# Performance work log

Hardware: AMD Instinct MI355X
Metric: run time of the kernel (lower is better)

Reference implementation:

```python
import jax, jax.numpy as jnp
import numpy as np

C = 768
HEADS = 12
NF = 8      # num_frames
SL = 196    # seq_len (patches per frame)
B = 2
N = 1 + NF * SL
HID = 4 * C


def _ln(x, g, b, eps=1e-5):
    mu = jnp.mean(x, axis=-1, keepdims=True)
    var = jnp.mean((x - mu) ** 2, axis=-1, keepdims=True)
    return (x - mu) * jax.lax.rsqrt(var + eps) * g + b


def setup_inputs() -> dict:
    key = jax.random.key(0)
    ks = jax.random.split(key, 16)
    s = 0.02
    return {
        "x": jax.random.normal(ks[0], (B, N, C), jnp.float32),
        "g1": jnp.ones((C,), jnp.float32),
        "b1": jnp.zeros((C,), jnp.float32),
        "Wqkv": jax.random.normal(ks[1], (C, 3 * C), jnp.float32) * s,
        "Wq": jax.random.normal(ks[2], (C, C), jnp.float32) * s,
        "Wkv": jax.random.normal(ks[3], (C, 2 * C), jnp.float32) * s,
        "Wp": jax.random.normal(ks[4], (C, C), jnp.float32) * s,
        "bp": jnp.zeros((C,), jnp.float32),
        "g2": jnp.ones((C,), jnp.float32),
        "b2": jnp.zeros((C,), jnp.float32),
        "W1": jax.random.normal(ks[5], (C, HID), jnp.float32) * s,
        "bf1": jnp.zeros((HID,), jnp.float32),
        "W2": jax.random.normal(ks[6], (HID, C), jnp.float32) * s,
        "bf2": jnp.zeros((C,), jnp.float32),
        "seq_len": SL,
        "num_frames": NF,
    }


def _traj_attn(xn, Wqkv, Wq, Wkv, Wp, bp, P, F):
    Bb, Nn, Cc = xn.shape
    h = HEADS
    d = Cc // h
    scale = d ** -0.5
    S = F * P  # non-cls tokens

    qkv = xn @ Wqkv                                   # (B,N,3C)
    q, k, v = jnp.split(qkv, 3, axis=-1)

    def heads(t):  # (B,N,C) -> (B*h, N, d)
        return t.reshape(Bb, Nn, h, d).transpose(0, 2, 1, 3).reshape(Bb * h, Nn, d)

    q, k, v = heads(q), heads(k), heads(v)
    cls_q, q_ = q[:, :1], q[:, 1:]
    k_ = k[:, 1:]
    v_ = v[:, 1:]

    # cls token attends to all tokens
    sim = jnp.einsum('bid,bjd->bij', cls_q * scale, k)
    cls_out = jnp.einsum('bij,bjd->bid', jax.nn.softmax(sim, axis=-1), v)
    cls_out = cls_out.reshape(Bb, h, 1, d).transpose(0, 2, 1, 3).reshape(Bb, 1, Cc)

    # stage 1: space-only softmax per frame
    qk = jnp.einsum('bqd,bkd->bqk', q_, k_).reshape(Bb * h, S, F, P)
    space_attn = jax.nn.softmax(scale * qk, axis=-1)          # (Bh,S,F,P)
    v_r = v_.reshape(Bb * h, F, P, d)
    x1 = jnp.einsum('bqfn,bfnd->bqfd', space_attn, v_r)       # (Bh,S,F,d)
    x1 = x1.reshape(Bb, h, S, F, d).transpose(0, 2, 3, 1, 4).reshape(Bb, S, F, Cc)

    # diagonal across (query-frame, key-frame)
    xg = x1.reshape(Bb, F, P, F, Cc)
    diag = jnp.diagonal(xg, axis1=1, axis2=3)                 # (B,P,C,F)
    x_diag = diag.transpose(0, 3, 1, 2).reshape(Bb, S, Cc)    # b (f n) d

    # stage 2: frame-wise attention
    q2 = (x_diag @ Wq).reshape(Bb, S, h, d).transpose(0, 2, 1, 3) * scale  # bhsd
    kv2 = x1 @ Wkv
    k2, v2 = jnp.split(kv2, 2, axis=-1)
    k2 = k2.reshape(Bb, S, F, h, d).transpose(0, 3, 1, 2, 4)  # bhsfd
    attn2 = jax.nn.softmax(jnp.einsum('bhsd,bhsfd->bhsf', q2, k2), axis=-1)
    xo = x1.reshape(Bb, S, F, h, d).transpose(0, 3, 1, 2, 4)  # use_original_code=True
    out = jnp.einsum('bhsf,bhsfd->bhsd', attn2, xo)
    out = out.transpose(0, 2, 1, 3).reshape(Bb, S, Cc)

    out = jnp.concatenate([cls_out, out], axis=1) @ Wp + bp
    return out


def reference(x, g1, b1, Wqkv, Wq, Wkv, Wp, bp, g2, b2, W1, bf1, W2, bf2, seq_len, num_frames):
    x = x + _traj_attn(_ln(x, g1, b1), Wqkv, Wq, Wkv, Wp, bp, seq_len, num_frames)
    h = _ln(x, g2, b2)
    h = jax.nn.gelu(h @ W1 + bf1, approximate=False) @ W2 + bf2
    return x + h
```

## Files before the change

kernel.cpp:

```cpp
#include <hip/hip_runtime.h>
#include <hip/hip_bf16.h>
#include <math.h>

#define C     768
#define HEADS 12
#define HD    64
#define NF    8
#define SL    196
#define BB    2
#define NN    1569
#define SS    1568
#define HID   3072
#define CLS_CH 256
#define CLS_NC 7
#define QSCALE 0.18033688011112042f

typedef __attribute__((ext_vector_type(8))) short short8;
typedef __attribute__((ext_vector_type(4))) float f32x4;
typedef unsigned short u16;

__device__ inline float fast_exp2(float x) { return __builtin_amdgcn_exp2f(x); }

__device__ inline u16 f2b(float f) {
    __hip_bfloat16 h = __float2bfloat16(f);
    return *reinterpret_cast<u16*>(&h);
}
__device__ inline float b2f(u16 u) {
    union { unsigned u; float f; } v; v.u = ((unsigned)u) << 16;
    return v.f;
}

__device__ inline void gload_lds16(const void* g, void* l) {
    __builtin_amdgcn_global_load_lds(
        (const __attribute__((address_space(1))) void*)g,
        (__attribute__((address_space(3))) void*)l, 16, 0, 0);
}

__global__ void ln_kernel(const float* __restrict__ x, const float* __restrict__ g,
                          const float* __restrict__ b, u16* __restrict__ out, int rows) {
    int row = blockIdx.x;
    if (row >= rows) return;
    const float* xr = x + (size_t)row * C;
    int tid = threadIdx.x;
    float v[3];
    float sum = 0.f, sumsq = 0.f;
#pragma unroll
    for (int i = 0; i < 3; i++) {
        v[i] = xr[tid + 256 * i];
        sum += v[i]; sumsq += v[i] * v[i];
    }
    __shared__ float s1[4], s2[4];
    for (int off = 32; off; off >>= 1) {
        sum   += __shfl_xor(sum, off);
        sumsq += __shfl_xor(sumsq, off);
    }
    int wave = tid >> 6, lane = tid & 63;
    if (lane == 0) { s1[wave] = sum; s2[wave] = sumsq; }
    __syncthreads();
    sum   = s1[0] + s1[1] + s1[2] + s1[3];
    sumsq = s2[0] + s2[1] + s2[2] + s2[3];
    float mu  = sum / C;
    float var = sumsq / C - mu * mu;
    float rstd = rsqrtf(fmaxf(var, 0.f) + 1e-5f);
    u16* outr = out + (size_t)row * C;
#pragma unroll
    for (int i = 0; i < 3; i++) {
        int c = tid + 256 * i;
        outr[c] = f2b((v[i] - mu) * rstd * g[c] + b[c]);
    }
}

__global__ void wtrans_kernel(const float* __restrict__ W, u16* __restrict__ Wt,
                              int K, int N, int ldb) {
    __shared__ float tile[64][65];
    int nb = blockIdx.x * 64, kb = blockIdx.y * 64;
    int tx = threadIdx.x & 63, ty = threadIdx.x >> 6;
#pragma unroll
    for (int i = 0; i < 64; i += 4)
        tile[ty + i][tx] = W[(size_t)(kb + ty + i) * ldb + nb + tx];
    __syncthreads();
#pragma unroll
    for (int i = 0; i < 64; i += 4)
        Wt[(size_t)(nb + ty + i) * K + kb + tx] = f2b(tile[tx][ty + i]);
}

template<int MODE, int BM, int BN>
__global__ __launch_bounds__(256) void gemm_bf16(
    const u16* __restrict__ A, const u16* __restrict__ Bt,
    const float* __restrict__ bias, const float* resid, void* Cout,
    int M, int N, int K, int lda, int ldb, int gx) {
    constexpr int MT   = BM / 32;
    constexpr int NT   = BN / 32;
    constexpr int ACH  = BM * 4;
    constexpr int TCH  = (BM + BN) * 4;
    constexpr int HALF = (BM + BN) * 64;
    __shared__ char smem[2 * HALF];
    int tid = threadIdx.x, lane = tid & 63, wave = tid >> 6;
    int wr = wave >> 1, wc = wave & 1;
    int r16 = lane & 15, kg = lane >> 4;

    int nwg = gridDim.x, orig = blockIdx.x;
    int qq = nwg >> 3, rr = nwg & 7, xcd = orig & 7, lid = orig >> 3;
    int wg = (xcd < rr ? xcd * (qq + 1) : rr * (qq + 1) + (xcd - rr) * qq) + lid;
    int bx = wg % gx, by = wg / gx;
    if constexpr (MODE == 4) {
        int mt_ = (M + BM - 1) / BM;
        int chunk = by / mt_; by -= chunk * mt_;
        A    += (size_t)chunk * K;
        Bt   += (size_t)chunk * K;
        Cout  = (void*)((float*)Cout + (size_t)chunk * ((size_t)M * N));
    }
    int row0 = by * BM, col0 = bx * BN;

    f32x4 acc[MT][NT];
#pragma unroll
    for (int mt = 0; mt < MT; mt++)
#pragma unroll
        for (int nt = 0; nt < NT; nt++) acc[mt][nt] = (f32x4){0.f, 0.f, 0.f, 0.f};

    auto stage = [&](char* dstbase, int ks) {
        int k0 = ks << 5;
#pragma unroll
        for (int it = 0; it < TCH / 256; it++) {
            int c = it * 256 + tid;
            const u16* src;
            if (c < ACH) {
                int ml = c >> 2, s = c & 3;
                int kgs = s ^ ((ml >> 1) & 3);
                int gm = row0 + ml; if (gm >= M) gm = M - 1;
                src = A + (size_t)gm * lda + k0 + kgs * 8;
            } else {
                int cc = c - ACH;
                int nl = cc >> 2, s = cc & 3;
                int kgs = s ^ ((nl >> 1) & 3);
                src = Bt + (size_t)(col0 + nl) * ldb + k0 + kgs * 8;
            }
            gload_lds16(src, dstbase + it * 4096 + wave * 1024);
        }
    };

    int nsteps = K >> 5;
    stage(smem, 0);
    __syncthreads();
    for (int ks = 0; ks < nsteps; ks++) {
        char* curb = smem + (ks & 1) * HALF;
        if (ks + 1 < nsteps) stage(smem + ((ks + 1) & 1) * HALF, ks + 1);
        short8 af[MT], bfr[NT];
#pragma unroll
        for (int mt = 0; mt < MT; mt++) {
            int ml = wr * (BM / 2) + mt * 16 + r16;
            af[mt] = *(const short8*)(curb + ml * 64 + ((kg ^ ((ml >> 1) & 3)) << 4));
        }
#pragma unroll
        for (int nt = 0; nt < NT; nt++) {
            int nl = wc * (BN / 2) + nt * 16 + r16;
            bfr[nt] = *(const short8*)(curb + BM * 64 + nl * 64 + ((kg ^ ((nl >> 1) & 3)) << 4));
        }
        __builtin_amdgcn_s_setprio(1);
#pragma unroll
        for (int mt = 0; mt < MT; mt++)
#pragma unroll
            for (int nt = 0; nt < NT; nt++)
                acc[mt][nt] = __builtin_amdgcn_mfma_f32_16x16x32_bf16(af[mt], bfr[nt], acc[mt][nt], 0, 0, 0);
        __builtin_amdgcn_s_setprio(0);
        __syncthreads();
    }
#pragma unroll
    for (int mt = 0; mt < MT; mt++) {
#pragma unroll
        for (int r2 = 0; r2 < 4; r2++) {
            int gm = row0 + wr * (BM / 2) + mt * 16 + kg * 4 + r2;
            if (gm >= M) continue;
#pragma unroll
            for (int nt = 0; nt < NT; nt++) {
                int gn = col0 + wc * (BN / 2) + nt * 16 + r16;
                float v = acc[mt][nt][r2];
                if constexpr (MODE == 1) {
                    v += bias[gn];
                    v = 0.5f * v * (1.f + erff(v * 0.70710678118f));
                }
                if constexpr (MODE == 2) {
                    v += bias[gn] + resid[(size_t)gm * N + gn];
                    ((float*)Cout)[(size_t)gm * N + gn] = v;
                } else if constexpr (MODE == 4) {
                    ((float*)Cout)[(size_t)gm * N + gn] = v;
                } else {
                    if constexpr (MODE == 3) { if (gn < 768) v *= QSCALE; }
                    ((u16*)Cout)[(size_t)gm * N + gn] = f2b(v);
                }
            }
        }
    }
}

__global__ void fc2_merge_kernel(const float* __restrict__ p,
                                 const float* __restrict__ bias, float* __restrict__ out) {
    int i = blockIdx.x * 256 + threadIdx.x;
    int total = BB * NN * (C / 4);
    if (i >= total) return;
    int c4 = i % (C / 4);
    size_t stride = (size_t)BB * NN * (C / 4);
    float4 bb = ((const float4*)bias)[c4];
    float4 a0 = ((const float4*)p)[i];
    float4 a1 = ((const float4*)p)[i + stride];
    float4 a2 = ((const float4*)p)[i + 2 * stride];
    float4 a3 = ((const float4*)p)[i + 3 * stride];
    float4 o  = ((float4*)out)[i];
    o.x += a0.x + a1.x + a2.x + a3.x + bb.x;
    o.y += a0.y + a1.y + a2.y + a3.y + bb.y;
    o.z += a0.z + a1.z + a2.z + a3.z + bb.z;
    o.w += a0.w + a1.w + a2.w + a3.w + bb.w;
    ((float4*)out)[i] = o;
}

__global__ void cls_partial_kernel(const u16* __restrict__ qkv, float* __restrict__ part) {
    int c = blockIdx.x, bh = blockIdx.y;
    int b = bh / HEADS, hh = bh % HEADS;
    int tid = threadIdx.x;
    int wave = tid >> 6, lane = tid & 63;
    __shared__ float s_q[HD];
    __shared__ float s_sc[CLS_CH];
    __shared__ float sm[4], ss[4];
    __shared__ float sacc[4][HD];
    if (tid < HD) s_q[tid] = b2f(qkv[(size_t)(b * NN) * 2304 + hh * HD + tid]);
    __syncthreads();

    int j0 = c * CLS_CH;
    int j = j0 + tid;
    float sc = -1e30f;
    if (j < NN) {
        const short8* kp = (const short8*)(qkv + ((size_t)(b * NN) + j) * 2304 + C + hh * HD);
        float acc = 0.f;
#pragma unroll
        for (int u = 0; u < 8; u++) {
            short8 kv = kp[u];
#pragma unroll
            for (int e = 0; e < 8; e++) acc += s_q[u * 8 + e] * b2f((u16)kv[e]);
        }
        sc = acc;
    }
    float m = sc;
    for (int off = 32; off; off >>= 1) m = fmaxf(m, __shfl_xor(m, off));
    if (lane == 0) sm[wave] = m;
    __syncthreads();
    m = fmaxf(fmaxf(sm[0], sm[1]), fmaxf(sm[2], sm[3]));
    float e = (j < NN) ? fast_exp2(sc - m) : 0.f;
    s_sc[tid] = e;
    float su = e;
    for (int off = 32; off; off >>= 1) su += __shfl_xor(su, off);
    if (lane == 0) ss[wave] = su;
    __syncthreads();
    float ssum = ss[0] + ss[1] + ss[2] + ss[3];

    int jj = tid >> 6, d = tid & 63;
    int jmax = NN - j0; if (jmax > CLS_CH) jmax = CLS_CH;
    const u16* vcol = qkv + ((size_t)(b * NN) + j0) * 2304 + 2 * C + hh * HD + d;
    float acc = 0.f;
    for (int t = jj; t < jmax; t += 4)
        acc += s_sc[t] * b2f(vcol[(size_t)t * 2304]);
    sacc[jj][d] = acc;
    __syncthreads();
    if (tid < HD) {
        float pv = sacc[0][tid] + sacc[1][tid] + sacc[2][tid] + sacc[3][tid];
        float* pp = part + ((size_t)bh * CLS_NC + c) * 66;
        pp[2 + tid] = pv;
        if (tid == 0) { pp[0] = m; pp[1] = ssum; }
    }
}

__global__ void cls_reduce_kernel(const float* __restrict__ part, u16* __restrict__ y) {
    int bh = blockIdx.x;
    int b = bh / HEADS, hh = bh % HEADS;
    int d = threadIdx.x;
    float gm = -1e30f;
#pragma unroll
    for (int c = 0; c < CLS_NC; c++)
        gm = fmaxf(gm, part[((size_t)bh * CLS_NC + c) * 66]);
    float tot = 0.f, pv = 0.f;
#pragma unroll
    for (int c = 0; c < CLS_NC; c++) {
        const float* pp = part + ((size_t)bh * CLS_NC + c) * 66;
        float w = fast_exp2(pp[0] - gm);
        tot += pp[1] * w;
        pv  += pp[2 + d] * w;
    }
    y[(size_t)(b * NN) * C + hh * HD + d] = f2b(pv / tot);
}

__global__ void repack_k_kernel(const u16* __restrict__ qkv, u16* __restrict__ Kb) {
    int t = blockIdx.x * 256 + threadIdx.x;
    if (t >= 24 * NF * 208 * 8) return;
    int d8 = t & 7;
    int rest = t >> 3;
    int n = rest % 208;
    rest /= 208;
    int f = rest % NF;
    int bh = rest / NF;
    int b = bh / HEADS, h = bh % HEADS;
    short8 v = {0, 0, 0, 0, 0, 0, 0, 0};
    if (n < SL)
        v = *(const short8*)(qkv + ((size_t)(b * NN) + 1 + f * SL + n) * 2304 + C + h * HD + d8 * 8);
    *(short8*)(Kb + (((size_t)bh * NF + f) * 208 + n) * 64 + d8 * 8) = v;
}

__global__ void repack_v_kernel(const u16* __restrict__ qkv, u16* __restrict__ Vt) {
    int t = blockIdx.x * 256 + threadIdx.x;
    if (t >= 24 * NF * 64 * 28) return;
    int n8 = t % 28;
    int rest = t / 28;
    int d = rest % 64;
    rest /= 64;
    int f = rest % NF;
    int bh = rest / NF;
    int b = bh / HEADS, h = bh % HEADS;
    int n0 = n8 * 8;
    const u16* src = qkv + ((size_t)(b * NN) + 1 + f * SL) * 2304 + 2 * C + h * HD + d;
    short8 v;
#pragma unroll
    for (int j = 0; j < 8; j++) {
        int n = n0 + j;
        v[j] = (n < SL) ? (short)src[(size_t)n * 2304] : (short)0;
    }
    *(short8*)(Vt + (((size_t)bh * NF + f) * 64 + d) * 224 + n0) = v;
}

__global__ void space_attn_mfma(
    const u16* __restrict__ qkv, const u16* __restrict__ Kb,
    const u16* __restrict__ Vt, u16* __restrict__ x1, u16* __restrict__ xd) {
    __shared__ u16 smem[14848];
    int tid = threadIdx.x;
    int lane = tid & 63, wave = tid >> 6;
    int r16 = lane & 15, kg = lane >> 4;

    int n = blockIdx.x;
    int xcd = n & 7;
    int slot = n >> 3;
    int j = slot % 25;
    int gw = slot / 25;
    int bh = xcd * 3 + gw % 3;
    int f = gw / 3;
    int b = bh / HEADS, h = bh % HEADS;

    int strip = j * 4 + wave;
    bool act = strip < 98;
    if (!act) strip = 97;
    int q0 = strip * 16;

    const u16* qrow = qkv + ((size_t)(b * NN) + 1 + q0 + r16) * 2304 + h * HD + kg * 8;
    short8 aq0 = *(const short8*)(qrow);
    short8 aq1 = *(const short8*)(qrow + 32);

    const char* kb_g = (const char*)(Kb + ((size_t)bh * NF + f) * 208 * 64);
    for (int w = wave; w < 26; w += 4) {
        int p = w * 1024 + lane * 16;
        int row = p >> 7;
        int src = (p & ~127) | ((p & 127) ^ ((row & 7) << 4));
        gload_lds16(kb_g + src, (char*)smem + p);
    }
    __syncthreads();

    f32x4 acc[13];
#pragma unroll
    for (int t = 0; t < 13; t++) acc[t] = (f32x4){0.f, 0.f, 0.f, 0.f};
    const char* ksm = (const char*)smem;
    int swz = (r16 & 7) << 4;
    __builtin_amdgcn_s_setprio(1);
#pragma unroll
    for (int t = 0; t < 13; t++) {
        const char* krow = ksm + (t * 16 + r16) * 128;
        short8 bk0 = *(const short8*)(krow + ((kg * 16) ^ swz));
        short8 bk1 = *(const short8*)(krow + ((64 + kg * 16) ^ swz));
        acc[t] = __builtin_amdgcn_mfma_f32_16x16x32_bf16(aq0, bk0, acc[t], 0, 0, 0);
        acc[t] = __builtin_amdgcn_mfma_f32_16x16x32_bf16(aq1, bk1, acc[t], 0, 0, 0);
    }
    __builtin_amdgcn_s_setprio(0);

    const u16* vbase = Vt + ((size_t)bh * NF + f) * 64 * 224;
    short8 vf[2][4];
#pragma unroll
    for (int dt = 0; dt < 4; dt++)
        vf[0][dt] = *(const short8*)(vbase + (dt * 16 + r16) * 224 + kg * 8);

    bool tail_mask = (r16 >= 4);
    float ssum[4] = {0.f, 0.f, 0.f, 0.f};
#pragma unroll
    for (int t = 0; t < 13; t++) {
#pragma unroll
        for (int r = 0; r < 4; r++) {
            float p = (t == 12 && tail_mask) ? 0.f : fast_exp2(acc[t][r]);
            acc[t][r] = p;
            ssum[r] += p;
        }
    }
#pragma unroll
    for (int off = 8; off; off >>= 1)
#pragma unroll
        for (int r = 0; r < 4; r++) ssum[r] += __shfl_xor(ssum[r], off);
    float inv[4];
#pragma unroll
    for (int r = 0; r < 4; r++) inv[r] = 1.f / ssum[r];

    __syncthreads();
    u16* pb = smem + wave * 3712;
#pragma unroll
    for (int t = 0; t < 13; t++)
#pragma unroll
        for (int r = 0; r < 4; r++)
            pb[(kg * 4 + r) * 232 + t * 16 + r16] = f2b(acc[t][r]);
    {
        int zr = lane >> 2, zc = 208 + (lane & 3) * 4;
        *(uint2*)(&pb[zr * 232 + zc]) = (uint2){0u, 0u};
    }

    f32x4 o[4];
#pragma unroll
    for (int dt = 0; dt < 4; dt++) o[dt] = (f32x4){0.f, 0.f, 0.f, 0.f};
    __builtin_amdgcn_s_setprio(1);
#pragma unroll
    for (int kc = 0; kc < 7; kc++) {
        if (kc < 6) {
#pragma unroll
            for (int dt = 0; dt < 4; dt++)
                vf[(kc + 1) & 1][dt] = *(const short8*)(vbase + (dt * 16 + r16) * 224 + (kc + 1) * 32 + kg * 8);
        }
        short8 pa = *(const short8*)(&pb[r16 * 232 + kc * 32 + kg * 8]);
#pragma unroll
        for (int dt = 0; dt < 4; dt++)
            o[dt] = __builtin_amdgcn_mfma_f32_16x16x32_bf16(pa, vf[kc & 1][dt], o[dt], 0, 0, 0);
    }
    __builtin_amdgcn_s_setprio(0);

    if (act) {
#pragma unroll
        for (int dt = 0; dt < 4; dt++)
#pragma unroll
            for (int r = 0; r < 4; r++) {
                int q = q0 + kg * 4 + r;
                u16 val = f2b(o[dt][r] * inv[r]);
                x1[(((size_t)(b * SS + q)) * NF + f) * C + h * HD + dt * 16 + r16] = val;
                if ((unsigned)(q - f * SL) < (unsigned)SL)
                    xd[((size_t)(b * SS + q)) * C + h * HD + dt * 16 + r16] = val;
            }
    }
}

__global__ void attn2_kernel(const u16* __restrict__ q2, const u16* __restrict__ k2,
                             const u16* __restrict__ x1, u16* __restrict__ y) {
    int item = blockIdx.x * 4 + (threadIdx.x >> 6);
    if (item >= BB * HEADS * SS) return;
    int lane = threadIdx.x & 63;
    int s = item % SS;
    int bh = item / SS;
    int b = bh / HEADS, hh = bh % HEADS;
    size_t rowbs = (size_t)(b * SS + s);
    float qv = b2f(q2[rowbs * C + hh * HD + lane]) * QSCALE;
    float lg[NF];
#pragma unroll
    for (int f = 0; f < NF; f++) {
        float p = qv * b2f(k2[(rowbs * NF + f) * C + hh * HD + lane]);
        for (int off = 32; off; off >>= 1) p += __shfl_xor(p, off);
        lg[f] = p;
    }
    float m = lg[0];
#pragma unroll
    for (int f = 1; f < NF; f++) m = fmaxf(m, lg[f]);
    float sum = 0.f;
#pragma unroll
    for (int f = 0; f < NF; f++) { lg[f] = fast_exp2(lg[f] - m); sum += lg[f]; }
    float inv = 1.f / sum;
    float acc = 0.f;
#pragma unroll
    for (int f = 0; f < NF; f++) acc += lg[f] * b2f(x1[(rowbs * NF + f) * C + hh * HD + lane]);
    y[((size_t)(b * NN) + 1 + s) * C + hh * HD + lane] = f2b(acc * inv);
}

extern "C" void kernel_launch(void* const* d_in, const int* in_sizes, int n_in,
                              void* d_out, int out_size, void* d_ws, size_t ws_size,
                              hipStream_t stream) {
    const float* x    = (const float*)d_in[0];
    const float* g1   = (const float*)d_in[1];
    const float* b1   = (const float*)d_in[2];
    const float* Wqkv = (const float*)d_in[3];
    const float* Wq   = (const float*)d_in[4];
    const float* Wkv  = (const float*)d_in[5];
    const float* Wp   = (const float*)d_in[6];
    const float* bp   = (const float*)d_in[7];
    const float* g2   = (const float*)d_in[8];
    const float* b2_  = (const float*)d_in[9];
    const float* W1   = (const float*)d_in[10];
    const float* bf1  = (const float*)d_in[11];
    const float* W2   = (const float*)d_in[12];
    const float* bf2  = (const float*)d_in[13];
    float* out = (float*)d_out;

    u16* us     = (u16*)d_ws;
    u16* xn_b   = us;
    u16* qkv_b  = xn_b   + 2409984;
    u16* Wt_qkv = qkv_b  + 7229952;
    u16* Wt_q   = Wt_qkv + 1769472;
    u16* Wt_kv  = Wt_q   + 589824;
    u16* Wt_p   = Wt_kv  + 589824;
    u16* W1t    = Wt_p   + 589824;
    u16* W2t    = W1t    + 2359296;
    u16* Kb     = W2t    + 2359296;
    u16* Vt     = Kb     + 2555904;
    u16* x1b    = Vt     + 2752512;
    u16* xdb    = x1b    + 19267584;
    u16* q2b    = xdb    + 2408448;
    u16* k2b    = q2b    + 2408448;
    u16* y_b    = k2b    + 19267584;
    u16* a1b    = y_b    + 2409984;
    float* cls_ws   = (float*)(a1b + 9639936);
    float* fc2_part = cls_ws + 24 * 7 * 66;

    const int M1 = BB * NN;
    const int M2 = BB * SS;
    const int M3 = BB * SS * NF;

    wtrans_kernel<<<dim3(2304 / 64, 768 / 64), 256, 0, stream>>>(Wqkv, Wt_qkv, 768, 2304, 2304);
    wtrans_kernel<<<dim3(768 / 64, 768 / 64), 256, 0, stream>>>(Wq, Wt_q, 768, 768, 768);
    wtrans_kernel<<<dim3(768 / 64, 768 / 64), 256, 0, stream>>>(Wkv, Wt_kv, 768, 768, 1536);
    wtrans_kernel<<<dim3(768 / 64, 768 / 64), 256, 0, stream>>>(Wp, Wt_p, 768, 768, 768);
    wtrans_kernel<<<dim3(3072 / 64, 768 / 64), 256, 0, stream>>>(W1, W1t, 768, 3072, 3072);
    wtrans_kernel<<<dim3(768 / 64, 3072 / 64), 256, 0, stream>>>(W2, W2t, 3072, 768, 768);
    ln_kernel<<<M1, 256, 0, stream>>>(x, g1, b1, xn_b, M1);
    gemm_bf16<3, 128, 64><<<36 * 25, 256, 0, stream>>>(
        xn_b, Wt_qkv, nullptr, nullptr, qkv_b, M1, 2304, 768, 768, 768, 36);
    repack_k_kernel<<<(24 * NF * 208 * 8 + 255) / 256, 256, 0, stream>>>(qkv_b, Kb);
    repack_v_kernel<<<(24 * NF * 64 * 28 + 255) / 256, 256, 0, stream>>>(qkv_b, Vt);
    cls_partial_kernel<<<dim3(CLS_NC, BB * HEADS), 256, 0, stream>>>(qkv_b, cls_ws);
    cls_reduce_kernel<<<BB * HEADS, 64, 0, stream>>>(cls_ws, y_b);
    space_attn_mfma<<<4800, 256, 0, stream>>>(qkv_b, Kb, Vt, x1b, xdb);
    gemm_bf16<0, 64, 64><<<12 * 49, 256, 0, stream>>>(
        xdb, Wt_q, nullptr, nullptr, q2b, M2, 768, 768, 768, 768, 12);
    gemm_bf16<0, 128, 128><<<6 * 196, 256, 0, stream>>>(
        x1b, Wt_kv, nullptr, nullptr, k2b, M3, 768, 768, 768, 768, 6);
    attn2_kernel<<<(BB * HEADS * SS + 3) / 4, 256, 0, stream>>>(q2b, k2b, x1b, y_b);
    gemm_bf16<2, 64, 64><<<12 * 50, 256, 0, stream>>>(
        y_b, Wt_p, bp, x, out, M1, 768, 768, 768, 768, 12);
    ln_kernel<<<M1, 256, 0, stream>>>(out, g2, b2_, xn_b, M1);
    gemm_bf16<1, 128, 64><<<48 * 25, 256, 0, stream>>>(
        xn_b, W1t, bf1, nullptr, a1b, M1, 3072, 768, 768, 768, 48);
    gemm_bf16<4, 128, 64><<<12 * 25 * 4, 256, 0, stream>>>(
        a1b, W2t, nullptr, nullptr, fc2_part, M1, 768, 768, 3072, 3072, 12);
    fc2_merge_kernel<<<(BB * NN * (C / 4) + 255) / 256, 256, 0, stream>>>(
        fc2_part, bf2, out);
}
```

Baseline: 309.5 us.

## Merge weight-transpose and repack launches; stage space-attention output through LDS

The six weight-transpose launches become one kernel that dispatches on block index, and the K and V repack kernels are merged into a single launch, cutting launch overhead. In the space-attention kernel, probabilities are written to shared memory inside the exp loop instead of being kept in registers, which should lower register pressure. The output tile is staged through LDS so x1 and xd are written as 16-byte rows instead of scattered 2-byte stores. The merged kernels branch on block index, and the extra LDS round trip adds a little latency in exchange for coalesced global writes.

```diff
diff --git a/kernel.cpp b/kernel.cpp
--- a/kernel.cpp
+++ b/kernel.cpp
@@ -70,10 +70,21 @@
     }
 }
 
-__global__ void wtrans_kernel(const float* __restrict__ W, u16* __restrict__ Wt,
-                              int K, int N, int ldb) {
+__global__ void wtrans_all_kernel(
+    const float* __restrict__ Wqkv, const float* __restrict__ Wq,
+    const float* __restrict__ Wkv,  const float* __restrict__ Wp,
+    const float* __restrict__ W1,   const float* __restrict__ W2,
+    u16* Tqkv, u16* Tq, u16* Tkv, u16* Tp, u16* T1, u16* T2) {
     __shared__ float tile[64][65];
-    int nb = blockIdx.x * 64, kb = blockIdx.y * 64;
+    int bid = blockIdx.x;
+    const float* W; u16* Wt; int K, ldb, gx;
+    if (bid < 432)       { W = Wqkv; Wt = Tqkv; K = 768;  ldb = 2304; gx = 36; }
+    else if (bid < 576)  { W = Wq;   Wt = Tq;   K = 768;  ldb = 768;  gx = 12; bid -= 432; }
+    else if (bid < 720)  { W = Wkv;  Wt = Tkv;  K = 768;  ldb = 1536; gx = 12; bid -= 576; }
+    else if (bid < 864)  { W = Wp;   Wt = Tp;   K = 768;  ldb = 768;  gx = 12; bid -= 720; }
+    else if (bid < 1440) { W = W1;   Wt = T1;   K = 768;  ldb = 3072; gx = 48; bid -= 864; }
+    else                 { W = W2;   Wt = T2;   K = 3072; ldb = 768;  gx = 12; bid -= 1440; }
+    int nb = (bid % gx) * 64, kb = (bid / gx) * 64;
     int tx = threadIdx.x & 63, ty = threadIdx.x >> 6;
 #pragma unroll
     for (int i = 0; i < 64; i += 4)
@@ -287,41 +298,43 @@
     y[(size_t)(b * NN) * C + hh * HD + d] = f2b(pv / tot);
 }
 
-__global__ void repack_k_kernel(const u16* __restrict__ qkv, u16* __restrict__ Kb) {
+__global__ void repack_kv_kernel(const u16* __restrict__ qkv,
+                                 u16* __restrict__ Kb, u16* __restrict__ Vt) {
+    const int NK = 24 * NF * 208 * 8;
+    const int NV = 24 * NF * 64 * 28;
     int t = blockIdx.x * 256 + threadIdx.x;
-    if (t >= 24 * NF * 208 * 8) return;
-    int d8 = t & 7;
-    int rest = t >> 3;
-    int n = rest % 208;
-    rest /= 208;
-    int f = rest % NF;
-    int bh = rest / NF;
-    int b = bh / HEADS, h = bh % HEADS;
-    short8 v = {0, 0, 0, 0, 0, 0, 0, 0};
-    if (n < SL)
-        v = *(const short8*)(qkv + ((size_t)(b * NN) + 1 + f * SL + n) * 2304 + C + h * HD + d8 * 8);
-    *(short8*)(Kb + (((size_t)bh * NF + f) * 208 + n) * 64 + d8 * 8) = v;
-}
-
-__global__ void repack_v_kernel(const u16* __restrict__ qkv, u16* __restrict__ Vt) {
-    int t = blockIdx.x * 256 + threadIdx.x;
-    if (t >= 24 * NF * 64 * 28) return;
-    int n8 = t % 28;
-    int rest = t / 28;
-    int d = rest % 64;
-    rest /= 64;
-    int f = rest % NF;
-    int bh = rest / NF;
-    int b = bh / HEADS, h = bh % HEADS;
-    int n0 = n8 * 8;
-    const u16* src = qkv + ((size_t)(b * NN) + 1 + f * SL) * 2304 + 2 * C + h * HD + d;
-    short8 v;
-#pragma unroll
-    for (int j = 0; j < 8; j++) {
-        int n = n0 + j;
-        v[j] = (n < SL) ? (short)src[(size_t)n * 2304] : (short)0;
-    }
-    *(short8*)(Vt + (((size_t)bh * NF + f) * 64 + d) * 224 + n0) = v;
+    if (t < NK) {
+        int d8 = t & 7;
+        int rest = t >> 3;
+        int n = rest % 208;
+        rest /= 208;
+        int f = rest % NF;
+        int bh = rest / NF;
+        int b = bh / HEADS, h = bh % HEADS;
+        short8 v = {0, 0, 0, 0, 0, 0, 0, 0};
+        if (n < SL)
+            v = *(const short8*)(qkv + ((size_t)(b * NN) + 1 + f * SL + n) * 2304 + C + h * HD + d8 * 8);
+        *(short8*)(Kb + (((size_t)bh * NF + f) * 208 + n) * 64 + d8 * 8) = v;
+    } else {
+        int u = t - NK;
+        if (u >= NV) return;
+        int n8 = u % 28;
+        int rest = u / 28;
+        int d = rest % 64;
+        rest /= 64;
+        int f = rest % NF;
+        int bh = rest / NF;
+        int b = bh / HEADS, h = bh % HEADS;
+        int n0 = n8 * 8;
+        const u16* src = qkv + ((size_t)(b * NN) + 1 + f * SL) * 2304 + 2 * C + h * HD + d;
+        short8 v;
+#pragma unroll
+        for (int jj = 0; jj < 8; jj++) {
+            int n = n0 + jj;
+            v[jj] = (n < SL) ? (short)src[(size_t)n * 2304] : (short)0;
+        }
+        *(short8*)(Vt + (((size_t)bh * NF + f) * 64 + d) * 224 + n0) = v;
+    }
 }
 
 __global__ void space_attn_mfma(
@@ -381,6 +394,9 @@
     for (int dt = 0; dt < 4; dt++)
         vf[0][dt] = *(const short8*)(vbase + (dt * 16 + r16) * 224 + kg * 8);
 
+    __syncthreads();
+    u16* pb = smem + wave * 3712;
+
     bool tail_mask = (r16 >= 4);
     float ssum[4] = {0.f, 0.f, 0.f, 0.f};
 #pragma unroll
@@ -388,29 +404,21 @@
 #pragma unroll
         for (int r = 0; r < 4; r++) {
             float p = (t == 12 && tail_mask) ? 0.f : fast_exp2(acc[t][r]);
-            acc[t][r] = p;
             ssum[r] += p;
-        }
-    }
-#pragma unroll
-    for (int off = 8; off; off >>= 1)
-#pragma unroll
-        for (int r = 0; r < 4; r++) ssum[r] += __shfl_xor(ssum[r], off);
-    float inv[4];
-#pragma unroll
-    for (int r = 0; r < 4; r++) inv[r] = 1.f / ssum[r];
-
-    __syncthreads();
-    u16* pb = smem + wave * 3712;
-#pragma unroll
-    for (int t = 0; t < 13; t++)
-#pragma unroll
-        for (int r = 0; r < 4; r++)
-            pb[(kg * 4 + r) * 232 + t * 16 + r16] = f2b(acc[t][r]);
+            pb[(kg * 4 + r) * 232 + t * 16 + r16] = f2b(p);
+        }
+    }
     {
         int zr = lane >> 2, zc = 208 + (lane & 3) * 4;
         *(uint2*)(&pb[zr * 232 + zc]) = (uint2){0u, 0u};
     }
+#pragma unroll
+    for (int off = 8; off; off >>= 1)
+#pragma unroll
+        for (int r = 0; r < 4; r++) ssum[r] += __shfl_xor(ssum[r], off);
+    float inv[4];
+#pragma unroll
+    for (int r = 0; r < 4; r++) inv[r] = 1.f / ssum[r];
 
     f32x4 o[4];
 #pragma unroll
@@ -434,13 +442,20 @@
 #pragma unroll
         for (int dt = 0; dt < 4; dt++)
 #pragma unroll
-            for (int r = 0; r < 4; r++) {
-                int q = q0 + kg * 4 + r;
-                u16 val = f2b(o[dt][r] * inv[r]);
-                x1[(((size_t)(b * SS + q)) * NF + f) * C + h * HD + dt * 16 + r16] = val;
-                if ((unsigned)(q - f * SL) < (unsigned)SL)
-                    xd[((size_t)(b * SS + q)) * C + h * HD + dt * 16 + r16] = val;
-            }
+            for (int r = 0; r < 4; r++)
+                pb[(kg * 4 + r) * 72 + dt * 16 + r16] = f2b(o[dt][r] * inv[r]);
+        u16* x1row = x1 + (((size_t)(b * SS + q0)) * NF + f) * C + h * HD;
+        u16* xdrow = xd + ((size_t)(b * SS + q0)) * C + h * HD;
+        int fbase = f * SL;
+#pragma unroll
+        for (int it = 0; it < 2; it++) {
+            int c = it * 64 + lane;
+            int qr = c >> 3, c8 = c & 7;
+            short8 v8 = *(const short8*)(&pb[qr * 72 + c8 * 8]);
+            *(short8*)(x1row + (size_t)qr * (NF * C) + c8 * 8) = v8;
+            if ((unsigned)(q0 + qr - fbase) < (unsigned)SL)
+                *(short8*)(xdrow + (size_t)qr * C + c8 * 8) = v8;
+        }
     }
 }
 
@@ -517,17 +532,13 @@
     const int M2 = BB * SS;
     const int M3 = BB * SS * NF;
 
-    wtrans_kernel<<<dim3(2304 / 64, 768 / 64), 256, 0, stream>>>(Wqkv, Wt_qkv, 768, 2304, 2304);
-    wtrans_kernel<<<dim3(768 / 64, 768 / 64), 256, 0, stream>>>(Wq, Wt_q, 768, 768, 768);
-    wtrans_kernel<<<dim3(768 / 64, 768 / 64), 256, 0, stream>>>(Wkv, Wt_kv, 768, 768, 1536);
-    wtrans_kernel<<<dim3(768 / 64, 768 / 64), 256, 0, stream>>>(Wp, Wt_p, 768, 768, 768);
-    wtrans_kernel<<<dim3(3072 / 64, 768 / 64), 256, 0, stream>>>(W1, W1t, 768, 3072, 3072);
-    wtrans_kernel<<<dim3(768 / 64, 3072 / 64), 256, 0, stream>>>(W2, W2t, 3072, 768, 768);
+    wtrans_all_kernel<<<2016, 256, 0, stream>>>(Wqkv, Wq, Wkv, Wp, W1, W2,
+                                                Wt_qkv, Wt_q, Wt_kv, Wt_p, W1t, W2t);
     ln_kernel<<<M1, 256, 0, stream>>>(x, g1, b1, xn_b, M1);
     gemm_bf16<3, 128, 64><<<36 * 25, 256, 0, stream>>>(
         xn_b, Wt_qkv, nullptr, nullptr, qkv_b, M1, 2304, 768, 768, 768, 36);
-    repack_k_kernel<<<(24 * NF * 208 * 8 + 255) / 256, 256, 0, stream>>>(qkv_b, Kb);
-    repack_v_kernel<<<(24 * NF * 64 * 28 + 255) / 256, 256, 0, stream>>>(qkv_b, Vt);
+    repack_kv_kernel<<<(24 * NF * 208 * 8 + 24 * NF * 64 * 28 + 255) / 256, 256, 0, stream>>>(
+        qkv_b, Kb, Vt);
     cls_partial_kernel<<<dim3(CLS_NC, BB * HEADS), 256, 0, stream>>>(qkv_b, cls_ws);
     cls_reduce_kernel<<<BB * HEADS, 64, 0, stream>>>(cls_ws, y_b);
     space_attn_mfma<<<4800, 256, 0, stream>>>(qkv_b, Kb, Vt, x1b, xdb);
```

Result: faster. 295.7 us (-4.5%).
